# Optimization experiments

Hardware: AMD Instinct MI355X
Metric: run time of the kernel (lower is better)

Reference implementation:

```python
import jax, jax.numpy as jnp
import numpy as np

N_WIRES = 4
N_LAYERS = 3
EPS = 1e-5


def _rx(t):
    c = jnp.cos(t / 2).astype(jnp.complex64)
    s = jnp.sin(t / 2).astype(jnp.complex64)
    return jnp.stack([jnp.stack([c, -1j * s], -1), jnp.stack([-1j * s, c], -1)], -2)


def _ry(t):
    c = jnp.cos(t / 2).astype(jnp.complex64)
    s = jnp.sin(t / 2).astype(jnp.complex64)
    return jnp.stack([jnp.stack([c, -s], -1), jnp.stack([s, c], -1)], -2)


def _rz(t):
    e0 = jnp.exp(-1j * t.astype(jnp.complex64) / 2)
    e1 = jnp.exp(1j * t.astype(jnp.complex64) / 2)
    z = jnp.zeros_like(e0)
    return jnp.stack([jnp.stack([e0, z], -1), jnp.stack([z, e1], -1)], -2)


def _apply_1q(st, U, w, n=N_WIRES):
    # st: [B, 2^n]; U: [2,2] (shared) or [B,2,2] (per-sample)
    B = st.shape[0]
    a, c = 2 ** w, 2 ** (n - w - 1)
    st = st.reshape(B, a, 2, c)
    if U.ndim == 2:
        st = jnp.einsum('ij,bajc->baic', U, st)
    else:
        st = jnp.einsum('bij,bajc->baic', U, st)
    return st.reshape(B, -1)


def _apply_cnot(st, w, n=N_WIRES):
    # CNOT with control w, target w+1
    B = st.shape[0]
    a, c = 2 ** w, 2 ** (n - w - 2)
    st = st.reshape(B, a, 2, 2, c)
    st = jnp.stack([st[:, :, 0], jnp.flip(st[:, :, 1], axis=2)], axis=2)
    return st.reshape(B, -1)


def _expz(st, w, n=N_WIRES):
    B = st.shape[0]
    a, c = 2 ** w, 2 ** (n - w - 1)
    p = (st.real ** 2 + st.imag ** 2).reshape(B, a, 2, c)
    return (p[:, :, 0] - p[:, :, 1]).sum(axis=(1, 2))


def _circuit(vparams, feats):
    # feats: [B, n_wires] encoding angles; vparams: [L, n_wires, 3]
    B = feats.shape[0]
    st = jnp.zeros((B, 2 ** N_WIRES), jnp.complex64).at[:, 0].set(1.0)
    for w in range(N_WIRES):
        st = _apply_1q(st, _rx(feats[:, w]), w)
    for l in range(N_LAYERS):
        for w in range(N_WIRES):
            st = _apply_1q(st, _rx(vparams[l, w, 0]), w)
            st = _apply_1q(st, _ry(vparams[l, w, 1]), w)
            st = _apply_1q(st, _rz(vparams[l, w, 2]), w)
        for w in range(N_WIRES - 1):
            st = _apply_cnot(st, w)
    return jnp.stack([_expz(st, w) for w in range(N_WIRES)], axis=1)  # [B, n_wires]


def setup_inputs() -> dict:
    key = jax.random.key(0)
    ks = jax.random.split(key, 4)
    B = 65536
    x = jax.random.normal(ks[0], (B, 1, 28, 28), jnp.float32)
    W = jax.random.normal(ks[1], (16, N_WIRES), jnp.float32) * 0.25
    b = jax.random.normal(ks[2], (N_WIRES,), jnp.float32) * 0.1
    vparams = jax.random.normal(ks[3], (N_LAYERS, N_WIRES, 3), jnp.float32)
    gamma = jnp.ones((N_WIRES,), jnp.float32)
    beta = jnp.zeros((N_WIRES,), jnp.float32)
    return {"x": x, "W": W, "b": b, "vparams": vparams, "gamma": gamma, "beta": beta}


def reference(x, W, b, vparams, gamma, beta):
    B = x.shape[0]
    # avg_pool2d kernel=6 stride=6 on 28x28 -> 4x4 (floor mode drops last 4 rows/cols)
    pooled = x[:, :, :24, :24].reshape(B, 1, 4, 6, 4, 6).mean(axis=(3, 5))
    feats = pooled.reshape(B, 16) @ W + b  # [B, n_wires]
    out = _circuit(vparams, feats)  # [B, n_wires]
    # BatchNorm1d (training mode: biased batch stats)
    mu = out.mean(axis=0)
    var = out.var(axis=0)
    return (out - mu) / jnp.sqrt(var + EPS) * gamma + beta
```

## Files before the change

kernel.cpp:

```cpp
#include <hip/hip_runtime.h>
#include <math.h>


#define IMG_PER_BLOCK 16
#define IMG_F 784
#define IMG_F4 196
#define ROW_F4 6
#define STG_F4 144
#define STG_F 576
#define TOT4 (IMG_PER_BLOCK * STG_F4)
#define ACC_SETS 64

#define GLOAD16(g, l) __builtin_amdgcn_global_load_lds( \
    (const __attribute__((address_space(1))) void*)(g), \
    (__attribute__((address_space(3))) void*)(l), 16, 0, 0)

__global__ __launch_bounds__(256) void qfc_main(
    const float* __restrict__ x,
    const float* __restrict__ W,
    const float* __restrict__ bias,
    const float* __restrict__ vparams,
    float* __restrict__ out,
    double* __restrict__ acc,
    int B)
{
    __shared__ float  lds_img[IMG_PER_BLOCK * STG_F];
    __shared__ float2 Uc[256];
    __shared__ float  bsum[4], bsq[4];

    const int t   = threadIdx.x;
    const int blk = blockIdx.x;

    if (t < 4) { bsum[t] = 0.f; bsq[t] = 0.f; }

    {
        const float4* x4   = (const float4*)x;
        float4*       lds4 = (float4*)lds_img;
        const int wb = t & 192;
        #pragma unroll
        for (int k = 0; k < 9; ++k) {
            int q    = t + k * 256;
            int g    = q / STG_F4;
            int r4   = q - g * STG_F4;
            int row  = r4 / ROW_F4;
            int col4 = r4 - row * ROW_F4;
            int img  = blk * IMG_PER_BLOCK + g;
            float4*       ldst = lds4 + k * 256 + wb;
            const float4* src  = x4 + img * IMG_F4 + row * 7 + col4;
            if (img < B)
                GLOAD16(src, ldst);
        }
    }

    {
        const int j = t >> 4, i = t & 15;
        float ux = (i == j) ? 1.f : 0.f, uy = 0.f;
        for (int l = 0; l < 3; ++l) {
            for (int w = 0; w < 4; ++w) {
                const float* vp = vparams + (l * 4 + w) * 3;
                const int m = 8 >> w;
                float s, c;
                __sincosf(0.5f * vp[0], &s, &c);
                {
                    float ox = __shfl_xor(ux, m);
                    float oy = __shfl_xor(uy, m);
                    float nx = c * ux + s * oy;
                    float ny = c * uy - s * ox;
                    ux = nx; uy = ny;
                }
                __sincosf(0.5f * vp[1], &s, &c);
                {
                    float ox = __shfl_xor(ux, m);
                    float oy = __shfl_xor(uy, m);
                    float sg = (i & m) ? s : -s;
                    ux = c * ux + sg * ox;
                    uy = c * uy + sg * oy;
                }
                __sincosf(0.5f * vp[2], &s, &c);
                {
                    float sg = (i & m) ? s : -s;
                    float nx = ux * c - sg * uy;
                    float ny = uy * c + sg * ux;
                    ux = nx; uy = ny;
                }
            }
            for (int w = 0; w < 3; ++w) {
                int mc = 8 >> w, mt = 4 >> w;
                float ox = __shfl_xor(ux, mt);
                float oy = __shfl_xor(uy, mt);
                if (i & mc) { ux = ox; uy = oy; }
            }
        }
        int pc = __popc(j) & 3;
        float px, py;
        if (pc == 0)      { px =  ux; py =  uy; }
        else if (pc == 1) { px =  uy; py = -ux; }
        else if (pc == 2) { px = -ux; py = -uy; }
        else              { px = -uy; py =  ux; }
        Uc[t] = make_float2(px, py);
    }
    __syncthreads();

    float pv;
    {
        const int g = t >> 4, cell = t & 15;
        const int ci = cell >> 2, cj = cell & 3;
        const float* base = lds_img + g * STG_F + ci * 6 * 24 + cj * 6;
        float sum = 0.f;
        #pragma unroll
        for (int r = 0; r < 6; ++r) {
            const float2* p2 = (const float2*)(base + r * 24);
            float2 a = p2[0], b2 = p2[1], c2 = p2[2];
            sum += a.x + a.y + b2.x + b2.y + c2.x + c2.y;
        }
        pv = sum * (1.0f / 36.0f);
    }

    {
        const int g = t >> 4, i = t & 15;
        float f0 = bias[0], f1 = bias[1], f2 = bias[2], f3 = bias[3];
        #pragma unroll
        for (int k = 0; k < 16; ++k) {
            float p = __shfl(pv, (t & 48) | k, 64);
            f0 += p * W[k * 4 + 0];
            f1 += p * W[k * 4 + 1];
            f2 += p * W[k * 4 + 2];
            f3 += p * W[k * 4 + 3];
        }
        float c0, s0, c1, s1, c2, s2, c3, s3;
        __sincosf(0.5f * f0, &s0, &c0);
        __sincosf(0.5f * f1, &s1, &c1);
        __sincosf(0.5f * f2, &s2, &c2);
        __sincosf(0.5f * f3, &s3, &c3);
        float AB[4] = { c0 * c1, c0 * s1, s0 * c1, s0 * s1 };
        float CD[4] = { c2 * c3, c2 * s3, s2 * c3, s2 * s3 };
        float yx = 0.f, yy = 0.f;
        #pragma unroll
        for (int j = 0; j < 16; ++j) {
            float r = AB[j >> 2] * CD[j & 3];
            float2 u = Uc[j * 16 + i];
            yx += u.x * r;
            yy += u.y * r;
        }
        float q = yx * yx + yy * yy;
        #pragma unroll
        for (int d = 1; d <= 8; d <<= 1) {
            float o = __shfl_xor(q, d);
            q = (i & d) ? (o - q) : (o + q);
        }
        int img = blk * IMG_PER_BLOCK + g;
        if ((i == 1 || i == 2 || i == 4 || i == 8) && img < B) {
            int w = (i == 8) ? 0 : (i == 4) ? 1 : (i == 2) ? 2 : 3;
            out[img * 4 + w] = q;
            atomicAdd(&bsum[w], q);
            atomicAdd(&bsq[w],  q * q);
        }
    }
    __syncthreads();

    if (t < 4) {
        int s = blk & (ACC_SETS - 1);
        atomicAdd(&acc[s * 8 + t],     (double)bsum[t]);
        atomicAdd(&acc[s * 8 + 4 + t], (double)bsq[t]);
    }
}

__global__ __launch_bounds__(256) void qfc_bn(
    float* __restrict__ out,
    const double* __restrict__ acc,
    const float* __restrict__ gamma,
    const float* __restrict__ beta,
    int B)
{
    __shared__ double tot_s[8];
    __shared__ float  mu_s[4], sc_s[4], bt_s[4];
    const int t = threadIdx.x;
    if (t < 8) {
        double tot = 0.0;
        for (int s = 0; s < ACC_SETS; ++s) tot += acc[s * 8 + t];
        tot_s[t] = tot;
    }
    __syncthreads();
    if (t < 4) {
        double invB = 1.0 / (double)B;
        double mu   = tot_s[t] * invB;
        double var  = tot_s[4 + t] * invB - mu * mu;
        mu_s[t] = (float)mu;
        sc_s[t] = (float)(1.0 / sqrt(var + 1e-5)) * gamma[t];
        bt_s[t] = beta[t];
    }
    __syncthreads();
    int idx = blockIdx.x * blockDim.x + t;
    if (idx < B) {
        float4* o4 = (float4*)out;
        float4 v = o4[idx];
        v.x = (v.x - mu_s[0]) * sc_s[0] + bt_s[0];
        v.y = (v.y - mu_s[1]) * sc_s[1] + bt_s[1];
        v.z = (v.z - mu_s[2]) * sc_s[2] + bt_s[2];
        v.w = (v.w - mu_s[3]) * sc_s[3] + bt_s[3];
        o4[idx] = v;
    }
}

extern "C" void kernel_launch(void* const* d_in, const int* in_sizes, int n_in,
                              void* d_out, int out_size, void* d_ws, size_t ws_size,
                              hipStream_t stream) {
    const float* x       = (const float*)d_in[0];
    const float* W       = (const float*)d_in[1];
    const float* b       = (const float*)d_in[2];
    const float* vparams = (const float*)d_in[3];
    const float* gamma   = (const float*)d_in[4];
    const float* beta    = (const float*)d_in[5];
    float* out = (float*)d_out;
    const int B = in_sizes[0] / IMG_F;

    double* acc = (double*)d_ws;
    hipMemsetAsync(d_ws, 0, ACC_SETS * 8 * sizeof(double), stream);

    int nblk1 = (B + IMG_PER_BLOCK - 1) / IMG_PER_BLOCK;
    qfc_main<<<nblk1, 256, 0, stream>>>(x, W, b, vparams, out, acc, B);

    int nblk2 = (B + 255) / 256;
    qfc_bn<<<nblk2, 256, 0, stream>>>(out, acc, gamma, beta, B);
}
```

Measured before the change: 286.4 us.

## Use persistent blocks with double-buffered async LDS image loads

Replaces the one-block-per-16-images grid with a fixed grid of up to 512 persistent blocks. Each block loops over image sets and prefetches the next set into a second LDS buffer with global_load_lds while it computes the current one. The 4x4 circuit unitary is built once per block instead of once per 16 images. The global double atomics and the memset are replaced by per-block partial sums, which the BN kernel reduces in two stages. In exchange, LDS use doubles and waitcnt and barrier handling is manual, which could limit occupancy or hide ordering mistakes.

```diff
diff --git a/kernel.cpp b/kernel.cpp
--- a/kernel.cpp
+++ b/kernel.cpp
@@ -2,54 +2,59 @@
 #include <math.h>
 
 
-#define IMG_PER_BLOCK 16
+#define IMG_PER_SET 16
 #define IMG_F 784
 #define IMG_F4 196
+#define IMG_BYTES 3136
 #define ROW_F4 6
 #define STG_F4 144
 #define STG_F 576
-#define TOT4 (IMG_PER_BLOCK * STG_F4)
-#define ACC_SETS 64
+#define SET_F4 (IMG_PER_SET * STG_F4)
+#define SET_F  (IMG_PER_SET * STG_F)
+#define NBLOCKS 512
 
 #define GLOAD16(g, l) __builtin_amdgcn_global_load_lds( \
     (const __attribute__((address_space(1))) void*)(g), \
     (__attribute__((address_space(3))) void*)(l), 16, 0, 0)
 
-__global__ __launch_bounds__(256) void qfc_main(
+__global__ __launch_bounds__(256, 2) void qfc_main(
     const float* __restrict__ x,
     const float* __restrict__ W,
     const float* __restrict__ bias,
     const float* __restrict__ vparams,
     float* __restrict__ out,
     double* __restrict__ acc,
-    int B)
+    int B, int nsets_tot, int nblk, int nsets_blk)
 {
-    __shared__ float  lds_img[IMG_PER_BLOCK * STG_F];
+    __shared__ float  lds_img[2 * SET_F];
     __shared__ float2 Uc[256];
     __shared__ float  bsum[4], bsq[4];
 
     const int t   = threadIdx.x;
     const int blk = blockIdx.x;
+    const int wb  = t & 192;
+    const unsigned ADV = (unsigned)nblk * (unsigned)(IMG_PER_SET * IMG_BYTES);
 
     if (t < 4) { bsum[t] = 0.f; bsq[t] = 0.f; }
 
+    unsigned off[9];
+    #pragma unroll
+    for (int k = 0; k < 9; ++k) {
+        int q    = t + k * 256;
+        int g    = q / STG_F4;
+        int r4   = q - g * STG_F4;
+        int row  = r4 / ROW_F4;
+        int col4 = r4 - row * ROW_F4;
+        long img = (long)blk * IMG_PER_SET + g;
+        if (img >= B) img = B - 1;
+        off[k] = (unsigned)(img * IMG_BYTES + row * 112 + col4 * 16);
+    }
+
     {
-        const float4* x4   = (const float4*)x;
-        float4*       lds4 = (float4*)lds_img;
-        const int wb = t & 192;
+        float4* lds4 = (float4*)lds_img;
         #pragma unroll
-        for (int k = 0; k < 9; ++k) {
-            int q    = t + k * 256;
-            int g    = q / STG_F4;
-            int r4   = q - g * STG_F4;
-            int row  = r4 / ROW_F4;
-            int col4 = r4 - row * ROW_F4;
-            int img  = blk * IMG_PER_BLOCK + g;
-            float4*       ldst = lds4 + k * 256 + wb;
-            const float4* src  = x4 + img * IMG_F4 + row * 7 + col4;
-            if (img < B)
-                GLOAD16(src, ldst);
-        }
+        for (int k = 0; k < 9; ++k)
+            GLOAD16((const char*)x + off[k], lds4 + k * 256 + wb);
     }
 
     {
@@ -99,69 +104,93 @@
         else              { px = -uy; py =  ux; }
         Uc[t] = make_float2(px, py);
     }
-    __syncthreads();
-
-    float pv;
-    {
-        const int g = t >> 4, cell = t & 15;
-        const int ci = cell >> 2, cj = cell & 3;
-        const float* base = lds_img + g * STG_F + ci * 6 * 24 + cj * 6;
-        float sum = 0.f;
-        #pragma unroll
-        for (int r = 0; r < 6; ++r) {
-            const float2* p2 = (const float2*)(base + r * 24);
-            float2 a = p2[0], b2 = p2[1], c2 = p2[2];
-            sum += a.x + a.y + b2.x + b2.y + c2.x + c2.y;
+    asm volatile("s_waitcnt lgkmcnt(0)" ::: "memory");
+
+    for (int it = 0; it < nsets_blk; ++it) {
+        const int set = blk + it * nblk;
+        const bool adv = (set + nblk) < nsets_tot;
+
+        __builtin_amdgcn_s_barrier();
+
+        if (adv) {
+            float4* nbuf = (float4*)(lds_img + ((it + 1) & 1) * SET_F);
+            #pragma unroll
+            for (int k = 0; k < 9; ++k) {
+                off[k] += ADV;
+                GLOAD16((const char*)x + off[k], nbuf + k * 256 + wb);
+            }
+            asm volatile("s_waitcnt vmcnt(9)" ::: "memory");
+        } else {
+            asm volatile("s_waitcnt vmcnt(0)" ::: "memory");
         }
-        pv = sum * (1.0f / 36.0f);
-    }
-
-    {
-        const int g = t >> 4, i = t & 15;
-        float f0 = bias[0], f1 = bias[1], f2 = bias[2], f3 = bias[3];
-        #pragma unroll
-        for (int k = 0; k < 16; ++k) {
-            float p = __shfl(pv, (t & 48) | k, 64);
-            f0 += p * W[k * 4 + 0];
-            f1 += p * W[k * 4 + 1];
-            f2 += p * W[k * 4 + 2];
-            f3 += p * W[k * 4 + 3];
+
+        __builtin_amdgcn_s_barrier();
+
+        if (set < nsets_tot) {
+            const float* cbuf = lds_img + (it & 1) * SET_F;
+
+            float pv;
+            {
+                const int g = t >> 4, cell = t & 15;
+                const int ci = cell >> 2, cj = cell & 3;
+                const float* base = cbuf + g * STG_F + ci * 6 * 24 + cj * 6;
+                float sum = 0.f;
+                #pragma unroll
+                for (int r = 0; r < 6; ++r) {
+                    const float2* p2 = (const float2*)(base + r * 24);
+                    float2 a = p2[0], b2 = p2[1], c2 = p2[2];
+                    sum += a.x + a.y + b2.x + b2.y + c2.x + c2.y;
+                }
+                pv = sum * (1.0f / 36.0f);
+            }
+
+            {
+                const int g = t >> 4, i = t & 15;
+                float f0 = bias[0], f1 = bias[1], f2 = bias[2], f3 = bias[3];
+                #pragma unroll
+                for (int k = 0; k < 16; ++k) {
+                    float p = __shfl(pv, (t & 48) | k, 64);
+                    f0 += p * W[k * 4 + 0];
+                    f1 += p * W[k * 4 + 1];
+                    f2 += p * W[k * 4 + 2];
+                    f3 += p * W[k * 4 + 3];
+                }
+                float c0, s0, c1, s1, c2, s2, c3, s3;
+                __sincosf(0.5f * f0, &s0, &c0);
+                __sincosf(0.5f * f1, &s1, &c1);
+                __sincosf(0.5f * f2, &s2, &c2);
+                __sincosf(0.5f * f3, &s3, &c3);
+                float AB[4] = { c0 * c1, c0 * s1, s0 * c1, s0 * s1 };
+                float CD[4] = { c2 * c3, c2 * s3, s2 * c3, s2 * s3 };
+                float yx = 0.f, yy = 0.f;
+                #pragma unroll
+                for (int j = 0; j < 16; ++j) {
+                    float r = AB[j >> 2] * CD[j & 3];
+                    float2 u = Uc[j * 16 + i];
+                    yx += u.x * r;
+                    yy += u.y * r;
+                }
+                float q = yx * yx + yy * yy;
+                #pragma unroll
+                for (int d = 1; d <= 8; d <<= 1) {
+                    float o = __shfl_xor(q, d);
+                    q = (i & d) ? (o - q) : (o + q);
+                }
+                int img = set * IMG_PER_SET + g;
+                if ((i == 1 || i == 2 || i == 4 || i == 8) && img < B) {
+                    int w = (i == 8) ? 0 : (i == 4) ? 1 : (i == 2) ? 2 : 3;
+                    out[img * 4 + w] = q;
+                    atomicAdd(&bsum[w], q);
+                    atomicAdd(&bsq[w],  q * q);
+                }
+            }
         }
-        float c0, s0, c1, s1, c2, s2, c3, s3;
-        __sincosf(0.5f * f0, &s0, &c0);
-        __sincosf(0.5f * f1, &s1, &c1);
-        __sincosf(0.5f * f2, &s2, &c2);
-        __sincosf(0.5f * f3, &s3, &c3);
-        float AB[4] = { c0 * c1, c0 * s1, s0 * c1, s0 * s1 };
-        float CD[4] = { c2 * c3, c2 * s3, s2 * c3, s2 * s3 };
-        float yx = 0.f, yy = 0.f;
-        #pragma unroll
-        for (int j = 0; j < 16; ++j) {
-            float r = AB[j >> 2] * CD[j & 3];
-            float2 u = Uc[j * 16 + i];
-            yx += u.x * r;
-            yy += u.y * r;
-        }
-        float q = yx * yx + yy * yy;
-        #pragma unroll
-        for (int d = 1; d <= 8; d <<= 1) {
-            float o = __shfl_xor(q, d);
-            q = (i & d) ? (o - q) : (o + q);
-        }
-        int img = blk * IMG_PER_BLOCK + g;
-        if ((i == 1 || i == 2 || i == 4 || i == 8) && img < B) {
-            int w = (i == 8) ? 0 : (i == 4) ? 1 : (i == 2) ? 2 : 3;
-            out[img * 4 + w] = q;
-            atomicAdd(&bsum[w], q);
-            atomicAdd(&bsq[w],  q * q);
-        }
-    }
-    __syncthreads();
-
-    if (t < 4) {
-        int s = blk & (ACC_SETS - 1);
-        atomicAdd(&acc[s * 8 + t],     (double)bsum[t]);
-        atomicAdd(&acc[s * 8 + 4 + t], (double)bsq[t]);
+    }
+
+    __syncthreads();
+    if (t < 8) {
+        float v = (t < 4) ? bsum[t] : bsq[t - 4];
+        acc[blk * 8 + t] = (double)v;
     }
 }
 
@@ -170,14 +199,24 @@
     const double* __restrict__ acc,
     const float* __restrict__ gamma,
     const float* __restrict__ beta,
-    int B)
+    int B, int nblk)
 {
+    __shared__ double red[64];
     __shared__ double tot_s[8];
     __shared__ float  mu_s[4], sc_s[4], bt_s[4];
     const int t = threadIdx.x;
+    if (t < 64) {
+        const int c = t & 7;
+        double p = 0.0;
+        for (int sidx = t >> 3; sidx < nblk; sidx += 8)
+            p += acc[sidx * 8 + c];
+        red[t] = p;
+    }
+    __syncthreads();
     if (t < 8) {
         double tot = 0.0;
-        for (int s = 0; s < ACC_SETS; ++s) tot += acc[s * 8 + t];
+        #pragma unroll
+        for (int k = 0; k < 8; ++k) tot += red[t + 8 * k];
         tot_s[t] = tot;
     }
     __syncthreads();
@@ -215,11 +254,17 @@
     const int B = in_sizes[0] / IMG_F;
 
     double* acc = (double*)d_ws;
-    hipMemsetAsync(d_ws, 0, ACC_SETS * 8 * sizeof(double), stream);
-
-    int nblk1 = (B + IMG_PER_BLOCK - 1) / IMG_PER_BLOCK;
-    qfc_main<<<nblk1, 256, 0, stream>>>(x, W, b, vparams, out, acc, B);
+
+    int nsets_tot = (B + IMG_PER_SET - 1) / IMG_PER_SET;
+    int nblk = NBLOCKS;
+    if (nblk > nsets_tot) nblk = nsets_tot;
+    int maxblk = (int)(ws_size / (8 * sizeof(double)));
+    if (nblk > maxblk && maxblk > 0) nblk = maxblk;
+    int nsets_blk = (nsets_tot + nblk - 1) / nblk;
+
+    qfc_main<<<nblk, 256, 0, stream>>>(x, W, b, vparams, out, acc,
+                                       B, nsets_tot, nblk, nsets_blk);
 
     int nblk2 = (B + 255) / 256;
-    qfc_bn<<<nblk2, 256, 0, stream>>>(out, acc, gamma, beta, B);
+    qfc_bn<<<nblk2, 256, 0, stream>>>(out, acc, gamma, beta, B, nblk);
 }
```

Measured after the change: 302.0 us. 5.4% more time.

## Load pooling windows directly into registers instead of staging images through LDS

Applied to the files above, without the earlier changes.

Drops the global_load_lds staging of each image's 24x24 region into shared memory. Each thread now loads its own 6x6 pooling cell as twelve float4s straight into registers and picks the needed columns by parity. The aim is to cut the 36KB LDS footprint and the LDS read pass so more blocks fit per CU, with launch bounds raised to ask for 4 blocks per SM. The cost is 8 loaded columns per row instead of 6, and overlapping, less coalesced reads across threads.

```diff
diff --git a/kernel.cpp b/kernel.cpp
--- a/kernel.cpp
+++ b/kernel.cpp
@@ -4,18 +4,9 @@
 
 #define IMG_PER_BLOCK 16
 #define IMG_F 784
-#define IMG_F4 196
-#define ROW_F4 6
-#define STG_F4 144
-#define STG_F 576
-#define TOT4 (IMG_PER_BLOCK * STG_F4)
 #define ACC_SETS 64
 
-#define GLOAD16(g, l) __builtin_amdgcn_global_load_lds( \
-    (const __attribute__((address_space(1))) void*)(g), \
-    (__attribute__((address_space(3))) void*)(l), 16, 0, 0)
-
-__global__ __launch_bounds__(256) void qfc_main(
+__global__ __launch_bounds__(256, 4) void qfc_main(
     const float* __restrict__ x,
     const float* __restrict__ W,
     const float* __restrict__ bias,
@@ -24,7 +15,6 @@
     double* __restrict__ acc,
     int B)
 {
-    __shared__ float  lds_img[IMG_PER_BLOCK * STG_F];
     __shared__ float2 Uc[256];
     __shared__ float  bsum[4], bsq[4];
 
@@ -33,23 +23,19 @@
 
     if (t < 4) { bsum[t] = 0.f; bsq[t] = 0.f; }
 
-    {
-        const float4* x4   = (const float4*)x;
-        float4*       lds4 = (float4*)lds_img;
-        const int wb = t & 192;
-        #pragma unroll
-        for (int k = 0; k < 9; ++k) {
-            int q    = t + k * 256;
-            int g    = q / STG_F4;
-            int r4   = q - g * STG_F4;
-            int row  = r4 / ROW_F4;
-            int col4 = r4 - row * ROW_F4;
-            int img  = blk * IMG_PER_BLOCK + g;
-            float4*       ldst = lds4 + k * 256 + wb;
-            const float4* src  = x4 + img * IMG_F4 + row * 7 + col4;
-            if (img < B)
-                GLOAD16(src, ldst);
-        }
+    const int g = t >> 4, cell = t & 15;
+    const int ci = cell >> 2, cj = cell & 3;
+    int img = blk * IMG_PER_BLOCK + g;
+    const bool valid = (img < B);
+    if (!valid) img = 0;
+
+    const float* ibase = x + (long)img * IMG_F + (ci * 6) * 28 + ((6 * cj) & ~3);
+    float4 va[6], vb[6];
+    #pragma unroll
+    for (int r = 0; r < 6; ++r) {
+        const float4* rp = (const float4*)(ibase + r * 28);
+        va[r] = rp[0];
+        vb[r] = rp[1];
     }
 
     {
@@ -103,21 +89,19 @@
 
     float pv;
     {
-        const int g = t >> 4, cell = t & 15;
-        const int ci = cell >> 2, cj = cell & 3;
-        const float* base = lds_img + g * STG_F + ci * 6 * 24 + cj * 6;
+        const bool odd = (cj & 1);
         float sum = 0.f;
         #pragma unroll
         for (int r = 0; r < 6; ++r) {
-            const float2* p2 = (const float2*)(base + r * 24);
-            float2 a = p2[0], b2 = p2[1], c2 = p2[2];
-            sum += a.x + a.y + b2.x + b2.y + c2.x + c2.y;
+            float mid  = va[r].z + va[r].w + vb[r].x + vb[r].y;
+            float ends = odd ? (vb[r].z + vb[r].w) : (va[r].x + va[r].y);
+            sum += mid + ends;
         }
         pv = sum * (1.0f / 36.0f);
     }
 
     {
-        const int g = t >> 4, i = t & 15;
+        const int i = t & 15;
         float f0 = bias[0], f1 = bias[1], f2 = bias[2], f3 = bias[3];
         #pragma unroll
         for (int k = 0; k < 16; ++k) {
@@ -148,8 +132,7 @@
             float o = __shfl_xor(q, d);
             q = (i & d) ? (o - q) : (o + q);
         }
-        int img = blk * IMG_PER_BLOCK + g;
-        if ((i == 1 || i == 2 || i == 4 || i == 8) && img < B) {
+        if ((i == 1 || i == 2 || i == 4 || i == 8) && valid) {
             int w = (i == 8) ? 0 : (i == 4) ? 1 : (i == 2) ? 2 : 3;
             out[img * 4 + w] = q;
             atomicAdd(&bsum[w], q);
```

Measured after the change: 287.1 us. No clear change (+0.2%).
